# Optimization experiments

Hardware: AMD Instinct MI355X
Metric: run time of the kernel (lower is better)

## Reference

```python
import jax, jax.numpy as jnp
import numpy as np

B, CIN, CMID, COUT, H, W = 4, 64, 128, 128, 128, 128
K = 9  # 3x3 taps
EPS = 1e-5


def conv3x3(x, w, b):
    # standard 3x3 conv, stride 1, pad 1, NCHW / OIHW
    y = jax.lax.conv_general_dilated(x, w, (1, 1), ((1, 1), (1, 1)),
                                     dimension_numbers=('NCHW', 'OIHW', 'NCHW'))
    return y + b[None, :, None, None]


def deform_conv3x3(x, offset, w, b):
    # torchvision DeformConv2d semantics (v1, no mask), kernel 3, pad 1, stride 1.
    # offset: [B, 2*K, H, W] with per-tap (dy, dx) pairs.
    Bn, C, Hn, Wn = x.shape
    off = offset.reshape(Bn, K, 2, Hn, Wn)
    off_y, off_x = off[:, :, 0], off[:, :, 1]          # [B,K,H,W]
    ky = (jnp.arange(K) // 3).astype(x.dtype)          # tap row 0..2
    kx = (jnp.arange(K) % 3).astype(x.dtype)           # tap col 0..2
    # sampling positions: p = out_pos - pad + tap + offset
    py = jnp.arange(Hn, dtype=x.dtype)[None, None, :, None] - 1.0 + ky[None, :, None, None] + off_y
    px = jnp.arange(Wn, dtype=x.dtype)[None, None, None, :] - 1.0 + kx[None, :, None, None] + off_x
    y0 = jnp.floor(py); x0 = jnp.floor(px)
    wy1 = py - y0; wx1 = px - x0                       # bilinear fractions
    y0i = y0.astype(jnp.int32); x0i = x0.astype(jnp.int32)
    xf = x.reshape(Bn, C, Hn * Wn)

    def gather(iy, ix):
        valid = ((iy >= 0) & (iy < Hn) & (ix >= 0) & (ix < Wn)).astype(x.dtype)
        idx = jnp.clip(iy, 0, Hn - 1) * Wn + jnp.clip(ix, 0, Wn - 1)  # [B,K,H,W]
        g = jax.vmap(lambda xb, ib: xb[:, ib])(xf, idx)               # [B,C,K,H,W]
        return g, valid

    g00, v00 = gather(y0i, x0i)
    g01, v01 = gather(y0i, x0i + 1)
    g10, v10 = gather(y0i + 1, x0i)
    g11, v11 = gather(y0i + 1, x0i + 1)

    def wmul(g, v, wgt):
        return g * (v * wgt)[:, None]                  # broadcast over channel dim

    sampled = (wmul(g00, v00, (1 - wy1) * (1 - wx1)) +
               wmul(g01, v01, (1 - wy1) * wx1) +
               wmul(g10, v10, wy1 * (1 - wx1)) +
               wmul(g11, v11, wy1 * wx1))              # [B,C,K,H,W]
    out = jnp.einsum('bckhw,ock->bohw', sampled, w.reshape(w.shape[0], C, K))
    return out + b[None, :, None, None]


def batchnorm_relu(x, gamma, beta):
    # training-mode BN: batch statistics over (N,H,W), biased variance
    mean = jnp.mean(x, axis=(0, 2, 3), keepdims=True)
    var = jnp.mean(jnp.square(x - mean), axis=(0, 2, 3), keepdims=True)
    y = (x - mean) * jax.lax.rsqrt(var + EPS)
    return jax.nn.relu(y * gamma[None, :, None, None] + beta[None, :, None, None])


def setup_inputs() -> dict:
    key = jax.random.key(0)
    ks = jax.random.split(key, 13)
    s = 0.05  # small weights keep offsets small / sampling mostly in-bounds
    return {
        'x': jax.random.normal(ks[0], (B, CIN, H, W), jnp.float32),
        'w_off1': jax.random.normal(ks[1], (2 * K, CIN, 3, 3), jnp.float32) * s,
        'b_off1': jnp.zeros((2 * K,), jnp.float32),
        'w1': jax.random.normal(ks[2], (CMID, CIN, 3, 3), jnp.float32) * s,
        'b1': jax.random.normal(ks[3], (CMID,), jnp.float32) * s,
        'g1': jnp.ones((CMID,), jnp.float32),
        'be1': jnp.zeros((CMID,), jnp.float32),
        'w_off2': jax.random.normal(ks[4], (2 * K, CMID, 3, 3), jnp.float32) * s,
        'b_off2': jnp.zeros((2 * K,), jnp.float32),
        'w2': jax.random.normal(ks[5], (COUT, CMID, 3, 3), jnp.float32) * s,
        'b2': jax.random.normal(ks[6], (COUT,), jnp.float32) * s,
        'g2': jnp.ones((COUT,), jnp.float32),
        'be2': jnp.zeros((COUT,), jnp.float32),
    }


def reference(x, w_off1, b_off1, w1, b1, g1, be1, w_off2, b_off2, w2, b2, g2, be2):
    offset1 = conv3x3(x, w_off1, b_off1)
    out = deform_conv3x3(x, offset1, w1, b1)
    out = batchnorm_relu(out, g1, be1)
    offset2 = conv3x3(out, w_off2, b_off2)
    out = deform_conv3x3(out, offset2, w2, b2)
    out = batchnorm_relu(out, g2, be2)
    return out
```

## Files before the change

kernel.cpp:

```cpp
#include <hip/hip_runtime.h>
#include <hip/hip_bf16.h>

#define BB 4
#define H_ 128
#define W_ 128
#define HWP 16384
#define CIN1 64
#define CMID 128
#define KOFF 18

typedef short short8 __attribute__((ext_vector_type(8)));
typedef float floatx4 __attribute__((ext_vector_type(4)));

#define WS_AB   16
#define WS_CVT  288
#define CVT_TOTAL 4447396
#define WS_WF1  4447744
#define WS_WF2  4484608
#define WS_XT   4558336
#define WS_Y1   7835136
#define WS_Y1T  16223744
#define WS_XTL  18320896
#define WS_WFO1 20418048
#define WS_WFO2 20436480
#define WS_PART 21600000
#define WS_Y2   WS_Y1

#define R_X     0
#define R_WOFF1 4194304
#define R_BOFF1 4204672
#define R_W1    4204690
#define R_B1    4278418
#define R_G1    4278546
#define R_BE1   4278674
#define R_WOFF2 4278802
#define R_BOFF2 4299538
#define R_W2    4299556
#define R_B2    4447012
#define R_G2    4447140
#define R_BE2   4447268

struct SrcPtrs { const void* p[13]; };

__device__ inline short f2bf(float f) {
    __hip_bfloat16 h = __float2bfloat16(f);
    return *reinterpret_cast<short*>(&h);
}
__device__ inline float bf2f(unsigned short u) {
    return __uint_as_float(((unsigned int)u) << 16);
}
__device__ inline float bfu_lo(unsigned int u) { return __uint_as_float(u << 16); }
__device__ inline float bfu_hi(unsigned int u) { return __uint_as_float(u & 0xFFFF0000u); }
__device__ inline float rl_f(float v, int i) {
    return __int_as_float(__builtin_amdgcn_readlane(__float_as_int(v), i));
}

__global__ void probe_dtype_k(const unsigned int* __restrict__ g1, int* __restrict__ flag) {
    if (threadIdx.x == 0 && blockIdx.x == 0) {
        flag[0] = ((g1[0] & 0xFFFFu) != 0u) ? 1 : 0;
    }
}

__global__ __launch_bounds__(256) void convert_inputs_k(SrcPtrs sp, float* __restrict__ dst,
                                                        const int* __restrict__ flag, int total) {
    int i = blockIdx.x * 256 + threadIdx.x;
    if (i >= total) return;
    constexpr int prefix[13] = {0, R_WOFF1, R_BOFF1, R_W1, R_B1, R_G1, R_BE1,
                                R_WOFF2, R_BOFF2, R_W2, R_B2, R_G2, R_BE2};
    const void* src = sp.p[0];
    int base = 0;
#pragma unroll
    for (int q = 1; q < 13; ++q) {
        if (i >= prefix[q]) { src = sp.p[q]; base = prefix[q]; }
    }
    int local = i - base;
    float v;
    if (flag[0] != 0) {
        v = bf2f(((const unsigned short*)src)[local]);
    } else {
        v = ((const float*)src)[local];
    }
    dst[i] = v;
}

template <int CIN>
__global__ __launch_bounds__(256) void wf_build_k(const float* __restrict__ w, short* __restrict__ wf) {
    constexpr int KSTEPS = CIN * 9 / 32;
    int idx = blockIdx.x * 256 + threadIdx.x;
    int j    = idx & 7;
    int lane = (idx >> 3) & 63;
    int rem  = idx >> 9;
    int ks   = rem % KSTEPS;
    int ct   = rem / KSTEPS;
    int co = ct * 16 + (lane & 15);
    int k  = ks * 32 + (lane >> 4) * 8 + j;
    int ci = k & (CIN - 1);
    int kk = k / CIN;
    wf[idx] = f2bf(w[(co * CIN + ci) * 9 + kk]);
}

template <int CIN>
__global__ __launch_bounds__(256) void wf_off_build_k(const float* __restrict__ w, short* __restrict__ wf) {
    constexpr int KSTEPS = CIN * 9 / 32;
    int idx = blockIdx.x * 256 + threadIdx.x;
    int j    = idx & 7;
    int lane = (idx >> 3) & 63;
    int rem  = idx >> 9;
    int ks   = rem % KSTEPS;
    int cc   = rem / KSTEPS;
    int sel  = cc >> 1;
    int co = (cc & 1) * 16 + (lane & 15);
    int k  = ks * 32 + (lane >> 4) * 8 + j;
    int ci = k & (CIN - 1);
    int kk = k / CIN;
    float v = (co < KOFF) ? w[(co * CIN + ci) * 9 + kk] : 0.f;
    short hi = f2bf(v);
    wf[idx] = sel ? f2bf(v - bf2f((unsigned short)hi)) : hi;
}

__global__ __launch_bounds__(256) void xt_build_k(const float* __restrict__ x,
                                                  unsigned short* __restrict__ xt,
                                                  unsigned short* __restrict__ xtl) {
    __shared__ __align__(4) short s_t[64 * 66];
    __shared__ __align__(4) short s_tl[64 * 66];
    int bi  = blockIdx.x;
    int hw0 = (bi & 255) * 64;
    int b   = bi >> 8;
    int t   = threadIdx.x;
    int hwp = t & 63;
#pragma unroll
    for (int it = 0; it < 16; ++it) {
        int c = it * 4 + (t >> 6);
        float v = x[((long)(b * 64 + c) << 14) + hw0 + hwp];
        short hi = f2bf(v);
        s_t[hwp * 66 + c]  = hi;
        s_tl[hwp * 66 + c] = f2bf(v - bf2f((unsigned short)hi));
    }
    __syncthreads();
#pragma unroll
    for (int it = 0; it < 8; ++it) {
        int i  = it * 256 + t;
        int c2 = (i & 31) * 2;
        int hw2 = i >> 5;
        long da = ((long)((b << 14) + hw0 + hw2)) * 64 + c2;
        *(int*)&xt[da]  = *(const int*)&s_t[hw2 * 66 + c2];
        *(int*)&xtl[da] = *(const int*)&s_tl[hw2 * 66 + c2];
    }
}

__device__ inline int conv_tpk(int h, int w0, int lane, int wv) {
    int tpk = 0;
    if (lane < 36) {
        int r = wv + 8 * lane;
        int p = r & 31;
        int k = r >> 5;
        int y = h - 1 + k / 3;
        int x = w0 + p - 1 + (k % 3);
        int valid = (y >= 0 && y < H_ && x >= 0 && x < W_) ? 1 : 0;
        int yc = min(max(y, 0), H_ - 1), xc = min(max(x, 0), W_ - 1);
        tpk = (yc * W_ + xc) | (valid << 16);
    }
    return tpk;
}

__device__ inline void convgather64(const unsigned short* __restrict__ xb, short* __restrict__ s_samp,
                                    int half, int li, int wv, int tpk) {
    constexpr int PADc = 584;
    unsigned int ub[18];
#pragma unroll
    for (int j = 0; j < 18; ++j) {
        int pkA = __builtin_amdgcn_readlane(tpk, 2 * j);
        int pkB = __builtin_amdgcn_readlane(tpk, 2 * j + 1);
        int pk = half ? pkB : pkA;
        unsigned int u = *(const unsigned int*)(xb + (pk & 0xFFFF) * 64 + 2 * li);
        ub[j] = (pk >> 16) ? u : 0u;
    }
#pragma unroll
    for (int j = 0; j < 18; ++j) {
        int r = wv + 8 * (half ? (2 * j + 1) : (2 * j));
        *(unsigned int*)&s_samp[(r & 31) * PADc + (r >> 5) * 64 + 2 * li] = ub[j];
    }
}

template <int I0, int NJ, int KKB>
__device__ inline void convgather128(const unsigned short* __restrict__ xb, short* __restrict__ s_samp,
                                     int lane, int wv, int tpk) {
    constexpr int PADc = 648;
    unsigned int ub[NJ];
#pragma unroll
    for (int j = 0; j < NJ; ++j) {
        int pk = __builtin_amdgcn_readlane(tpk, I0 + j);
        unsigned int u = *(const unsigned int*)(xb + (pk & 0xFFFF) * 128 + 2 * lane);
        ub[j] = (pk >> 16) ? u : 0u;
    }
#pragma unroll
    for (int j = 0; j < NJ; ++j) {
        int r = wv + 8 * (I0 + j);
        *(unsigned int*)&s_samp[(r & 31) * PADc + ((r >> 5) - KKB) * 128 + 2 * lane] = ub[j];
    }
}

__device__ inline void build_table2_lds(const float* __restrict__ s_off,
                                        int h, int w0, int lane, int wv,
                                        int& tpk, float& tw0, float& tw1, float& tw2, float& tw3) {
    tpk = 0; tw0 = tw1 = tw2 = tw3 = 0.f;
    if (lane < 36) {
        int r = wv + 8 * lane;
        int p = r & 31;
        int k = r >> 5;
        int wpix = w0 + p;
        float oy = s_off[(2 * k) * 32 + p];
        float ox = s_off[(2 * k + 1) * 32 + p];
        float py = (float)(h - 1 + (k / 3)) + oy;
        float px = (float)(wpix - 1 + (k % 3)) + ox;
        float fy = floorf(py), fx = floorf(px);
        float wy = py - fy, wx = px - fx;
        int y0 = (int)fy, x0 = (int)fx;
        int y1 = y0 + 1, x1 = x0 + 1;
        bool vy0 = (y0 >= 0) && (y0 < H_);
        bool vy1 = (y1 >= 0) && (y1 < H_);
        bool vx0 = (x0 >= 0) && (x0 < W_);
        bool vx1 = (x1 >= 0) && (x1 < W_);
        float wy0 = 1.f - wy, wx0 = 1.f - wx;
        tw0 = (vy0 && vx0) ? wy0 * wx0 : 0.f;
        tw1 = (vy0 && vx1) ? wy0 * wx  : 0.f;
        tw2 = (vy1 && vx0) ? wy  * wx0 : 0.f;
        tw3 = (vy1 && vx1) ? wy  * wx  : 0.f;
        int iy0 = min(max(y0, 0), H_ - 1), iy1 = min(max(y1, 0), H_ - 1);
        int ix0 = min(max(x0, 0), W_ - 1), ix1 = min(max(x1, 0), W_ - 1);
        int dx = ix1 - ix0;
        int dy = iy1 - iy0;
        tpk = (iy0 * W_ + ix0) | (dx << 14) | (dy << 15);
    }
}

template <int NB>
__device__ inline void gather_batch128v2(const unsigned short* __restrict__ xb, short* __restrict__ s_samp,
                                         int i0, int kkbase, int wv, int lane,
                                         int tpk, float tw0, float tw1, float tw2, float tw3) {
    constexpr int PADc = 648;
    uint4 ub[NB];
#pragma unroll
    for (int j = 0; j < NB; ++j) {
        int pk = __builtin_amdgcn_readlane(tpk, i0 + j);
        const unsigned short* b00 = xb + (pk & 0x3FFF) * 128;
        const unsigned short* b01 = b00 + ((pk >> 14) & 1) * 128;
        const unsigned short* b10 = b00 + ((pk >> 15) & 1) * (W_ * 128);
        const unsigned short* b11 = b01 + ((pk >> 15) & 1) * (W_ * 128);
        ub[j].x = *(const unsigned int*)(b00 + 2 * lane);
        ub[j].y = *(const unsigned int*)(b01 + 2 * lane);
        ub[j].z = *(const unsigned int*)(b10 + 2 * lane);
        ub[j].w = *(const unsigned int*)(b11 + 2 * lane);
    }
#pragma unroll
    for (int j = 0; j < NB; ++j) {
        int i = i0 + j;
        int r = wv + 8 * i;
        float w00 = rl_f(tw0, i), w01 = rl_f(tw1, i), w10 = rl_f(tw2, i), w11 = rl_f(tw3, i);
        float vlo = w00 * bfu_lo(ub[j].x) + w01 * bfu_lo(ub[j].y)
                  + w10 * bfu_lo(ub[j].z) + w11 * bfu_lo(ub[j].w);
        float vhi = w00 * bfu_hi(ub[j].x) + w01 * bfu_hi(ub[j].y)
                  + w10 * bfu_hi(ub[j].z) + w11 * bfu_hi(ub[j].w);
        __hip_bfloat162 h2 = __float22bfloat162_rn(make_float2(vlo, vhi));
        *(unsigned int*)&s_samp[(r & 31) * PADc + ((r >> 5) - kkbase) * 128 + 2 * lane] =
            *reinterpret_cast<unsigned int*>(&h2);
    }
}

template <int NBP>
__device__ inline void gather_batch64v2(const unsigned short* __restrict__ xb, short* __restrict__ s_samp,
                                        int i0, int wv, int half, int li,
                                        int tpk, float tw0, float tw1, float tw2, float tw3) {
    constexpr int PADc = 584;
    uint4 ub[NBP];
#pragma unroll
    for (int j = 0; j < NBP; ++j) {
        int iA = i0 + 2 * j, iB = iA + 1;
        int pkA = __builtin_amdgcn_readlane(tpk, iA);
        int pkB = __builtin_amdgcn_readlane(tpk, iB);
        int pk = half ? pkB : pkA;
        const unsigned short* b00 = xb + (pk & 0x3FFF) * 64;
        const unsigned short* b01 = b00 + ((pk >> 14) & 1) * 64;
        const unsigned short* b10 = b00 + ((pk >> 15) & 1) * (W_ * 64);
        const unsigned short* b11 = b01 + ((pk >> 15) & 1) * (W_ * 64);
        ub[j].x = *(const unsigned int*)(b00 + 2 * li);
        ub[j].y = *(const unsigned int*)(b01 + 2 * li);
        ub[j].z = *(const unsigned int*)(b10 + 2 * li);
        ub[j].w = *(const unsigned int*)(b11 + 2 * li);
    }
#pragma unroll
    for (int j = 0; j < NBP; ++j) {
        int iA = i0 + 2 * j, iB = iA + 1;
        float w00 = half ? rl_f(tw0, iB) : rl_f(tw0, iA);
        float w01 = half ? rl_f(tw1, iB) : rl_f(tw1, iA);
        float w10 = half ? rl_f(tw2, iB) : rl_f(tw2, iA);
        float w11 = half ? rl_f(tw3, iB) : rl_f(tw3, iA);
        float vlo = w00 * bfu_lo(ub[j].x) + w01 * bfu_lo(ub[j].y)
                  + w10 * bfu_lo(ub[j].z) + w11 * bfu_lo(ub[j].w);
        float vhi = w00 * bfu_hi(ub[j].x) + w01 * bfu_hi(ub[j].y)
                  + w10 * bfu_hi(ub[j].z) + w11 * bfu_hi(ub[j].w);
        __hip_bfloat162 h2 = __float22bfloat162_rn(make_float2(vlo, vhi));
        int r = wv + 8 * (half ? iB : iA);
        *(unsigned int*)&s_samp[(r & 31) * PADc + (r >> 5) * 64 + 2 * li] =
            *reinterpret_cast<unsigned int*>(&h2);
    }
}

__global__ __launch_bounds__(512, 4) void fused64_k(const unsigned short* __restrict__ xt,
                                                    const unsigned short* __restrict__ xtl,
                                                    const short* __restrict__ wfo,
                                                    const float* __restrict__ boff,
                                                    const short* __restrict__ wf,
                                                    const float* __restrict__ bias,
                                                    float* __restrict__ out) {
    constexpr int KSTEPS = 18;
    constexpr int PADc = 584;
    __shared__ __align__(16) short s_samp[32 * PADc];
    __shared__ float s_red[4 * 256];
    __shared__ float s_off[KOFF * 32];

    int bi = blockIdx.x;
    int w0 = (bi & 3) * 32;
    int h  = (bi >> 2) & 127;
    int b  = bi >> 9;
    int t  = threadIdx.x;
    int lane = t & 63;
    int wv   = t >> 6;

    const unsigned short* xbh = xt  + (long)b * HWP * 64;
    const unsigned short* xbl = xtl + (long)b * HWP * 64;
    int half = lane >> 5, li = lane & 31;
    int p_   = lane & 15;
    int quad = lane >> 4;

    {
        int tpkc = conv_tpk(h, w0, lane, wv);
        int c   = wv & 3;
        int ksl = wv >> 2;
        int ct  = c & 1;
        int pt  = c >> 1;
        int row = pt * 16 + p_;
        floatx4 acc;
#pragma unroll
        for (int r = 0; r < 4; ++r) {
            int co = ct * 16 + quad * 4 + r;
            acc[r] = (ksl == 0 && co < KOFF) ? boff[co] : 0.f;
        }

        convgather64(xbh, s_samp, half, li, wv, tpkc);
        __syncthreads();
#pragma unroll
        for (int ki = 0; ki < 9; ++ki) {
            int ks = ksl * 9 + ki;
            short8 bfr = *(const short8*)&s_samp[row * PADc + ks * 32 + quad * 8];
            short8 ah  = *(const short8*)&wfo[(((long)ct * KSTEPS + ks) * 64 + lane) * 8];
            short8 al  = *(const short8*)&wfo[(((long)(2 + ct) * KSTEPS + ks) * 64 + lane) * 8];
            acc = __builtin_amdgcn_mfma_f32_16x16x32_bf16(ah, bfr, acc, 0, 0, 0);
            acc = __builtin_amdgcn_mfma_f32_16x16x32_bf16(al, bfr, acc, 0, 0, 0);
        }
        __syncthreads();

        convgather64(xbl, s_samp, half, li, wv, tpkc);
        __syncthreads();
#pragma unroll
        for (int ki = 0; ki < 9; ++ki) {
            int ks = ksl * 9 + ki;
            short8 bfr = *(const short8*)&s_samp[row * PADc + ks * 32 + quad * 8];
            short8 ah  = *(const short8*)&wfo[(((long)ct * KSTEPS + ks) * 64 + lane) * 8];
            acc = __builtin_amdgcn_mfma_f32_16x16x32_bf16(ah, bfr, acc, 0, 0, 0);
        }

        if (ksl == 1) {
#pragma unroll
            for (int r = 0; r < 4; ++r) s_red[c * 256 + (quad * 4 + r) * 16 + p_] = acc[r];
        }
        __syncthreads();
        if (ksl == 0) {
#pragma unroll
            for (int r = 0; r < 4; ++r) {
                int co = ct * 16 + quad * 4 + r;
                if (co < KOFF) {
                    s_off[co * 32 + pt * 16 + p_] = acc[r] + s_red[c * 256 + (quad * 4 + r) * 16 + p_];
                }
            }
        }
        __syncthreads();
    }

    int tpk; float tw0, tw1, tw2, tw3;
    build_table2_lds(s_off, h, w0, lane, wv, tpk, tw0, tw1, tw2, tw3);

    gather_batch64v2<6>(xbh, s_samp,  0, wv, half, li, tpk, tw0, tw1, tw2, tw3);
    gather_batch64v2<6>(xbh, s_samp, 12, wv, half, li, tpk, tw0, tw1, tw2, tw3);
    gather_batch64v2<6>(xbh, s_samp, 24, wv, half, li, tpk, tw0, tw1, tw2, tw3);
    __syncthreads();

    int ct = wv;
    floatx4 acc0, acc1;
#pragma unroll
    for (int r = 0; r < 4; ++r) {
        float bv = bias[ct * 16 + quad * 4 + r];
        acc0[r] = bv;
        acc1[r] = bv;
    }
#pragma unroll 3
    for (int ks = 0; ks < KSTEPS; ++ks) {
        short8 a  = *(const short8*)&wf[(((long)ct * KSTEPS + ks) * 64 + lane) * 8];
        short8 b0 = *(const short8*)&s_samp[p_ * PADc + ks * 32 + quad * 8];
        short8 b1 = *(const short8*)&s_samp[(16 + p_) * PADc + ks * 32 + quad * 8];
        acc0 = __builtin_amdgcn_mfma_f32_16x16x32_bf16(a, b0, acc0, 0, 0, 0);
        acc1 = __builtin_amdgcn_mfma_f32_16x16x32_bf16(a, b1, acc1, 0, 0, 0);
    }

    long ob = ((long)(b * 128) << 14) + (h << 7) + w0 + p_;
#pragma unroll
    for (int r = 0; r < 4; ++r) {
        long cpl = (long)(ct * 16 + quad * 4 + r) << 14;
        out[ob + cpl]      = acc0[r];
        out[ob + 16 + cpl] = acc1[r];
    }
}

__global__ __launch_bounds__(512, 4) void fused128_k(const unsigned short* __restrict__ xt,
                                                     const unsigned short* __restrict__ xtl,
                                                     const short* __restrict__ wfo,
                                                     const float* __restrict__ boff,
                                                     const short* __restrict__ wf,
                                                     const float* __restrict__ bias,
                                                     float* __restrict__ out) {
    constexpr int KSTEPS = 36;
    constexpr int PADc = 648;
    __shared__ __align__(16) short s_samp[32 * PADc];
    __shared__ float s_red[4 * 256];
    __shared__ float s_off[KOFF * 32];

    int bi = blockIdx.x;
    int w0 = (bi & 3) * 32;
    int h  = (bi >> 2) & 127;
    int b  = bi >> 9;
    int t  = threadIdx.x;
    int lane = t & 63;
    int wv   = t >> 6;

    const unsigned short* xbh = xt  + (long)b * HWP * 128;
    const unsigned short* xbl = xtl + (long)b * HWP * 128;
    int p_   = lane & 15;
    int quad = lane >> 4;

    {
        int tpkc = conv_tpk(h, w0, lane, wv);
        int c   = wv & 3;
        int ksl = wv >> 2;
        int ct  = c & 1;
        int pt  = c >> 1;
        int row = pt * 16 + p_;
        floatx4 acc;
#pragma unroll
        for (int r = 0; r < 4; ++r) {
            int co = ct * 16 + quad * 4 + r;
            acc[r] = (ksl == 0 && co < KOFF) ? boff[co] : 0.f;
        }

        convgather128<0, 16, 0>(xbh, s_samp, lane, wv, tpkc);
        __syncthreads();
#pragma unroll
        for (int ki = 0; ki < 8; ++ki) {
            int ks = ksl * 8 + ki;
            short8 bfr = *(const short8*)&s_samp[row * PADc + ks * 32 + quad * 8];
            short8 ah  = *(const short8*)&wfo[(((long)ct * KSTEPS + ks) * 64 + lane) * 8];
            short8 al  = *(const short8*)&wfo[(((long)(2 + ct) * KSTEPS + ks) * 64 + lane) * 8];
            acc = __builtin_amdgcn_mfma_f32_16x16x32_bf16(ah, bfr, acc, 0, 0, 0);
            acc = __builtin_amdgcn_mfma_f32_16x16x32_bf16(al, bfr, acc, 0, 0, 0);
        }
        __syncthreads();

        convgather128<16, 20, 4>(xbh, s_samp, lane, wv, tpkc);
        __syncthreads();
#pragma unroll
        for (int ki = 0; ki < 10; ++ki) {
            int ks = 16 + ksl * 10 + ki;
            short8 bfr = *(const short8*)&s_samp[row * PADc + (ks - 16) * 32 + quad * 8];
            short8 ah  = *(const short8*)&wfo[(((long)ct * KSTEPS + ks) * 64 + lane) * 8];
            short8 al  = *(const short8*)&wfo[(((long)(2 + ct) * KSTEPS + ks) * 64 + lane) * 8];
            acc = __builtin_amdgcn_mfma_f32_16x16x32_bf16(ah, bfr, acc, 0, 0, 0);
            acc = __builtin_amdgcn_mfma_f32_16x16x32_bf16(al, bfr, acc, 0, 0, 0);
        }
        __syncthreads();

        convgather128<0, 16, 0>(xbl, s_samp, lane, wv, tpkc);
        __syncthreads();
#pragma unroll
        for (int ki = 0; ki < 8; ++ki) {
            int ks = ksl * 8 + ki;
            short8 bfr = *(const short8*)&s_samp[row * PADc + ks * 32 + quad * 8];
            short8 ah  = *(const short8*)&wfo[(((long)ct * KSTEPS + ks) * 64 + lane) * 8];
            acc = __builtin_amdgcn_mfma_f32_16x16x32_bf16(ah, bfr, acc, 0, 0, 0);
        }
        __syncthreads();

        convgather128<16, 20, 4>(xbl, s_samp, lane, wv, tpkc);
        __syncthreads();
#pragma unroll
        for (int ki = 0; ki < 10; ++ki) {
            int ks = 16 + ksl * 10 + ki;
            short8 bfr = *(const short8*)&s_samp[row * PADc + (ks - 16) * 32 + quad * 8];
            short8 ah  = *(const short8*)&wfo[(((long)ct * KSTEPS + ks) * 64 + lane) * 8];
            acc = __builtin_amdgcn_mfma_f32_16x16x32_bf16(ah, bfr, acc, 0, 0, 0);
        }

        if (ksl == 1) {
#pragma unroll
            for (int r = 0; r < 4; ++r) s_red[c * 256 + (quad * 4 + r) * 16 + p_] = acc[r];
        }
        __syncthreads();
        if (ksl == 0) {
#pragma unroll
            for (int r = 0; r < 4; ++r) {
                int co = ct * 16 + quad * 4 + r;
                if (co < KOFF) {
                    s_off[co * 32 + pt * 16 + p_] = acc[r] + s_red[c * 256 + (quad * 4 + r) * 16 + p_];
                }
            }
        }
        __syncthreads();
    }

    int tpk; float tw0, tw1, tw2, tw3;
    build_table2_lds(s_off, h, w0, lane, wv, tpk, tw0, tw1, tw2, tw3);

    int ct = wv;
    floatx4 acc0, acc1;
#pragma unroll
    for (int r = 0; r < 4; ++r) {
        float bv = bias[ct * 16 + quad * 4 + r];
        acc0[r] = bv;
        acc1[r] = bv;
    }

    gather_batch128v2<8>(xbh, s_samp, 0, 0, wv, lane, tpk, tw0, tw1, tw2, tw3);
    gather_batch128v2<8>(xbh, s_samp, 8, 0, wv, lane, tpk, tw0, tw1, tw2, tw3);
    __syncthreads();
#pragma unroll 4
    for (int ks = 0; ks < 16; ++ks) {
        short8 a  = *(const short8*)&wf[(((long)ct * KSTEPS + ks) * 64 + lane) * 8];
        short8 b0 = *(const short8*)&s_samp[p_ * PADc + ks * 32 + quad * 8];
        short8 b1 = *(const short8*)&s_samp[(16 + p_) * PADc + ks * 32 + quad * 8];
        acc0 = __builtin_amdgcn_mfma_f32_16x16x32_bf16(a, b0, acc0, 0, 0, 0);
        acc1 = __builtin_amdgcn_mfma_f32_16x16x32_bf16(a, b1, acc1, 0, 0, 0);
    }
    __syncthreads();

    gather_batch128v2<5>(xbh, s_samp, 16, 4, wv, lane, tpk, tw0, tw1, tw2, tw3);
    gather_batch128v2<5>(xbh, s_samp, 21, 4, wv, lane, tpk, tw0, tw1, tw2, tw3);
    gather_batch128v2<5>(xbh, s_samp, 26, 4, wv, lane, tpk, tw0, tw1, tw2, tw3);
    gather_batch128v2<5>(xbh, s_samp, 31, 4, wv, lane, tpk, tw0, tw1, tw2, tw3);
    __syncthreads();
#pragma unroll 4
    for (int ks = 16; ks < KSTEPS; ++ks) {
        short8 a  = *(const short8*)&wf[(((long)ct * KSTEPS + ks) * 64 + lane) * 8];
        short8 b0 = *(const short8*)&s_samp[p_ * PADc + (ks - 16) * 32 + quad * 8];
        short8 b1 = *(const short8*)&s_samp[(16 + p_) * PADc + (ks - 16) * 32 + quad * 8];
        acc0 = __builtin_amdgcn_mfma_f32_16x16x32_bf16(a, b0, acc0, 0, 0, 0);
        acc1 = __builtin_amdgcn_mfma_f32_16x16x32_bf16(a, b1, acc1, 0, 0, 0);
    }

    long ob = ((long)(b * 128) << 14) + (h << 7) + w0 + p_;
#pragma unroll
    for (int r = 0; r < 4; ++r) {
        long cpl = (long)(ct * 16 + quad * 4 + r) << 14;
        out[ob + cpl]      = acc0[r];
        out[ob + 16 + cpl] = acc1[r];
    }
}

__global__ __launch_bounds__(256) void bn_stats_part_k(const float* __restrict__ y, float* __restrict__ part) {
    int bi = blockIdx.x;
    int c = bi & 127;
    int b = bi >> 7;
    int t = threadIdx.x;
    const float4* p4 = (const float4*)(y + ((long)(b * 128 + c) << 14));
    float sum = 0.f, ss = 0.f;
#pragma unroll
    for (int i = 0; i < 16; ++i) {
        float4 v = p4[t + 256 * i];
        sum += v.x + v.y + v.z + v.w;
        ss  += v.x * v.x + v.y * v.y + v.z * v.z + v.w * v.w;
    }
#pragma unroll
    for (int o = 32; o > 0; o >>= 1) { sum += __shfl_down(sum, o); ss += __shfl_down(ss, o); }
    __shared__ float s1[4], s2[4];
    int wave = t >> 6;
    if ((t & 63) == 0) { s1[wave] = sum; s2[wave] = ss; }
    __syncthreads();
    if (t == 0) {
        part[bi]       = s1[0] + s1[1] + s1[2] + s1[3];
        part[512 + bi] = s2[0] + s2[1] + s2[2] + s2[3];
    }
}

__global__ __launch_bounds__(256) void bn_apply_dual_k(float* __restrict__ y, const float* __restrict__ part,
                                                       const float* __restrict__ g, const float* __restrict__ be,
                                                       unsigned short* __restrict__ yt,
                                                       unsigned short* __restrict__ ytl) {
    __shared__ __align__(4) short s_t[64 * 134];
    __shared__ __align__(4) short s_tl[64 * 134];
    __shared__ float s_a[128], s_sh[128];
    int t = threadIdx.x;
    if (t < 128) {
        float sum = part[t] + part[128 + t] + part[256 + t] + part[384 + t];
        float ss  = part[512 + t] + part[640 + t] + part[768 + t] + part[896 + t];
        float mean = sum * (1.f / 65536.f);
        float var  = ss  * (1.f / 65536.f) - mean * mean;
        float inv  = rsqrtf(var + 1e-5f);
        float a = g[t] * inv;
        s_a[t]  = a;
        s_sh[t] = be[t] - mean * a;
    }
    __syncthreads();

    int bi  = blockIdx.x;
    int hw0 = (bi & 255) * 64;
    int b   = bi >> 8;
    int hwp = t & 63;
#pragma unroll 4
    for (int it = 0; it < 32; ++it) {
        int c = it * 4 + (t >> 6);
        float a = s_a[c], sh = s_sh[c];
        long addr = ((long)(b * 128 + c) << 14) + hw0 + hwp;
        float v = y[addr];
        v = fmaxf(v * a + sh, 0.f);
        y[addr] = v;
        short hi = f2bf(v);
        s_t[hwp * 134 + c]  = hi;
        s_tl[hwp * 134 + c] = f2bf(v - bf2f((unsigned short)hi));
    }
    __syncthreads();
#pragma unroll 4
    for (int it = 0; it < 16; ++it) {
        int i   = it * 256 + t;
        int c2  = (i & 63) * 2;
        int hw2 = i >> 6;
        long da = ((long)((b << 14) + hw0 + hw2)) * 128 + c2;
        *(int*)&yt[da]  = *(const int*)&s_t[hw2 * 134 + c2];
        *(int*)&ytl[da] = *(const int*)&s_tl[hw2 * 134 + c2];
    }
}

__global__ __launch_bounds__(256) void bn_apply_out_k(const float* __restrict__ y, const float* __restrict__ part,
                                                      const float* __restrict__ g, const float* __restrict__ be,
                                                      const int* __restrict__ flag, void* __restrict__ out, int total4) {
    __shared__ float s_a[128], s_sh[128];
    int t = threadIdx.x;
    if (t < 128) {
        float sum = part[t] + part[128 + t] + part[256 + t] + part[384 + t];
        float ss  = part[512 + t] + part[640 + t] + part[768 + t] + part[896 + t];
        float mean = sum * (1.f / 65536.f);
        float var  = ss  * (1.f / 65536.f) - mean * mean;
        float inv  = rsqrtf(var + 1e-5f);
        float a = g[t] * inv;
        s_a[t]  = a;
        s_sh[t] = be[t] - mean * a;
    }
    __syncthreads();

    int i = blockIdx.x * 256 + t;
    if (i >= total4) return;
    int c = (i >> 12) & 127;
    float a = s_a[c], sh = s_sh[c];
    float4 v = reinterpret_cast<const float4*>(y)[i];
    v.x = fmaxf(v.x * a + sh, 0.f);
    v.y = fmaxf(v.y * a + sh, 0.f);
    v.z = fmaxf(v.z * a + sh, 0.f);
    v.w = fmaxf(v.w * a + sh, 0.f);
    if (flag[0] != 0) {
        ushort4 u;
        u.x = (unsigned short)f2bf(v.x);
        u.y = (unsigned short)f2bf(v.y);
        u.z = (unsigned short)f2bf(v.z);
        u.w = (unsigned short)f2bf(v.w);
        reinterpret_cast<ushort4*>(out)[i] = u;
    } else {
        reinterpret_cast<float4*>(out)[i] = v;
    }
}

extern "C" void kernel_launch(void* const* d_in, const int* in_sizes, int n_in,
                              void* d_out, int out_size, void* d_ws, size_t ws_size,
                              hipStream_t stream) {
    float* ws   = (float*)d_ws;
    int*   flag = (int*)d_ws;
    float* cvt  = ws + WS_CVT;

    const float* X     = cvt + R_X;
    const float* Woff1 = cvt + R_WOFF1;
    const float* Boff1 = cvt + R_BOFF1;
    const float* W1f   = cvt + R_W1;
    const float* B1f   = cvt + R_B1;
    const float* G1    = cvt + R_G1;
    const float* Be1   = cvt + R_BE1;
    const float* Woff2 = cvt + R_WOFF2;
    const float* Boff2 = cvt + R_BOFF2;
    const float* W2f   = cvt + R_W2;
    const float* B2f   = cvt + R_B2;
    const float* G2    = cvt + R_G2;
    const float* Be2   = cvt + R_BE2;

    short* WF1  = (short*)(ws + WS_WF1);
    short* WF2  = (short*)(ws + WS_WF2);
    short* WFO1 = (short*)(ws + WS_WFO1);
    short* WFO2 = (short*)(ws + WS_WFO2);
    unsigned short* XT   = (unsigned short*)(ws + WS_XT);
    unsigned short* XTL  = (unsigned short*)(ws + WS_XTL);
    unsigned short* Y1T  = (unsigned short*)(ws + WS_Y1T);
    unsigned short* Y1TL = (unsigned short*)(ws + WS_CVT);
    float* PART = ws + WS_PART;
    float* Y1   = ws + WS_Y1;
    float* Y2   = ws + WS_Y2;

    SrcPtrs sp;
    for (int j = 0; j < 13; ++j) sp.p[j] = d_in[j];

    probe_dtype_k<<<1, 64, 0, stream>>>((const unsigned int*)d_in[5], flag);
    convert_inputs_k<<<(CVT_TOTAL + 255) / 256, 256, 0, stream>>>(sp, cvt, flag, CVT_TOTAL);
    wf_build_k<64><<<288, 256, 0, stream>>>(W1f, WF1);
    wf_build_k<128><<<576, 256, 0, stream>>>(W2f, WF2);
    wf_off_build_k<64><<<144, 256, 0, stream>>>(Woff1, WFO1);
    wf_off_build_k<128><<<288, 256, 0, stream>>>(Woff2, WFO2);
    xt_build_k<<<1024, 256, 0, stream>>>(X, XT, XTL);

    fused64_k<<<BB * 128 * 4, 512, 0, stream>>>(XT, XTL, WFO1, Boff1, WF1, B1f, Y1);
    bn_stats_part_k<<<512, 256, 0, stream>>>(Y1, PART);
    bn_apply_dual_k<<<1024, 256, 0, stream>>>(Y1, PART, G1, Be1, Y1T, Y1TL);

    fused128_k<<<BB * 128 * 4, 512, 0, stream>>>(Y1T, Y1TL, WFO2, Boff2, WF2, B2f, Y2);
    bn_stats_part_k<<<512, 256, 0, stream>>>(Y2, PART);
    bn_apply_out_k<<<(BB * 128 * HWP / 4 + 255) / 256, 256, 0, stream>>>(Y2, PART, G2, Be2, flag, d_out, BB * 128 * HWP / 4);
}
```

Baseline: 330.8 us.

## Fuse BN statistics into deform-conv epilogues and shrink LDS tiles for occupancy

Drops the separate BN statistics kernels. Each fused conv kernel now reduces per-channel sum and sum-of-squares with wave shuffles and accumulates them into a zeroed partials buffer via atomics. The K dimension of the staged samples is split into smaller chunks (PADc 520), so LDS per block shrinks and launch bounds can request 8 blocks per CU. It also removes the unused write-back of normalized Y1. The costs are extra syncs and gather phases, plus atomic contention on 256 addresses.

```diff
diff --git a/kernel.cpp b/kernel.cpp
--- a/kernel.cpp
+++ b/kernel.cpp
@@ -5,8 +5,6 @@
 #define H_ 128
 #define W_ 128
 #define HWP 16384
-#define CIN1 64
-#define CMID 128
 #define KOFF 18
 
 typedef short short8 __attribute__((ext_vector_type(8)));
@@ -163,29 +161,32 @@
     return tpk;
 }
 
+template <int J0, int NJ, int KKB>
 __device__ inline void convgather64(const unsigned short* __restrict__ xb, short* __restrict__ s_samp,
                                     int half, int li, int wv, int tpk) {
-    constexpr int PADc = 584;
-    unsigned int ub[18];
-#pragma unroll
-    for (int j = 0; j < 18; ++j) {
-        int pkA = __builtin_amdgcn_readlane(tpk, 2 * j);
-        int pkB = __builtin_amdgcn_readlane(tpk, 2 * j + 1);
+    constexpr int PADc = 520;
+    unsigned int ub[NJ];
+#pragma unroll
+    for (int j = 0; j < NJ; ++j) {
+        int jj = J0 + j;
+        int pkA = __builtin_amdgcn_readlane(tpk, 2 * jj);
+        int pkB = __builtin_amdgcn_readlane(tpk, 2 * jj + 1);
         int pk = half ? pkB : pkA;
         unsigned int u = *(const unsigned int*)(xb + (pk & 0xFFFF) * 64 + 2 * li);
         ub[j] = (pk >> 16) ? u : 0u;
     }
 #pragma unroll
-    for (int j = 0; j < 18; ++j) {
-        int r = wv + 8 * (half ? (2 * j + 1) : (2 * j));
-        *(unsigned int*)&s_samp[(r & 31) * PADc + (r >> 5) * 64 + 2 * li] = ub[j];
+    for (int j = 0; j < NJ; ++j) {
+        int jj = J0 + j;
+        int r = wv + 8 * (half ? (2 * jj + 1) : (2 * jj));
+        *(unsigned int*)&s_samp[(r & 31) * PADc + ((r >> 5) - KKB) * 64 + 2 * li] = ub[j];
     }
 }
 
 template <int I0, int NJ, int KKB>
 __device__ inline void convgather128(const unsigned short* __restrict__ xb, short* __restrict__ s_samp,
                                      int lane, int wv, int tpk) {
-    constexpr int PADc = 648;
+    constexpr int PADc = 520;
     unsigned int ub[NJ];
 #pragma unroll
     for (int j = 0; j < NJ; ++j) {
@@ -238,7 +239,7 @@
 __device__ inline void gather_batch128v2(const unsigned short* __restrict__ xb, short* __restrict__ s_samp,
                                          int i0, int kkbase, int wv, int lane,
                                          int tpk, float tw0, float tw1, float tw2, float tw3) {
-    constexpr int PADc = 648;
+    constexpr int PADc = 520;
     uint4 ub[NB];
 #pragma unroll
     for (int j = 0; j < NB; ++j) {
@@ -269,9 +270,9 @@
 
 template <int NBP>
 __device__ inline void gather_batch64v2(const unsigned short* __restrict__ xb, short* __restrict__ s_samp,
-                                        int i0, int wv, int half, int li,
+                                        int i0, int kkbase, int wv, int half, int li,
                                         int tpk, float tw0, float tw1, float tw2, float tw3) {
-    constexpr int PADc = 584;
+    constexpr int PADc = 520;
     uint4 ub[NBP];
 #pragma unroll
     for (int j = 0; j < NBP; ++j) {
@@ -301,20 +302,36 @@
                   + w10 * bfu_hi(ub[j].z) + w11 * bfu_hi(ub[j].w);
         __hip_bfloat162 h2 = __float22bfloat162_rn(make_float2(vlo, vhi));
         int r = wv + 8 * (half ? iB : iA);
-        *(unsigned int*)&s_samp[(r & 31) * PADc + (r >> 5) * 64 + 2 * li] =
+        *(unsigned int*)&s_samp[(r & 31) * PADc + ((r >> 5) - kkbase) * 64 + 2 * li] =
             *reinterpret_cast<unsigned int*>(&h2);
     }
 }
 
-__global__ __launch_bounds__(512, 4) void fused64_k(const unsigned short* __restrict__ xt,
+__device__ inline void bn_epilogue(floatx4 acc0, floatx4 acc1, int ct, int quad, int p_,
+                                   float* __restrict__ part) {
+#pragma unroll
+    for (int r = 0; r < 4; ++r) {
+        float sm = acc0[r] + acc1[r];
+        float sq = acc0[r] * acc0[r] + acc1[r] * acc1[r];
+#pragma unroll
+        for (int o = 1; o < 16; o <<= 1) { sm += __shfl_xor(sm, o); sq += __shfl_xor(sq, o); }
+        if (p_ == 0) {
+            int co = ct * 16 + quad * 4 + r;
+            atomicAdd(&part[co], sm);
+            atomicAdd(&part[512 + co], sq);
+        }
+    }
+}
+
+__global__ __launch_bounds__(512, 8) void fused64_k(const unsigned short* __restrict__ xt,
                                                     const unsigned short* __restrict__ xtl,
                                                     const short* __restrict__ wfo,
                                                     const float* __restrict__ boff,
                                                     const short* __restrict__ wf,
                                                     const float* __restrict__ bias,
-                                                    float* __restrict__ out) {
-    constexpr int KSTEPS = 18;
-    constexpr int PADc = 584;
+                                                    float* __restrict__ out,
+                                                    float* __restrict__ part) {
+    constexpr int PADc = 520;
     __shared__ __align__(16) short s_samp[32 * PADc];
     __shared__ float s_red[4 * 256];
     __shared__ float s_off[KOFF * 32];
@@ -347,26 +364,48 @@
             acc[r] = (ksl == 0 && co < KOFF) ? boff[co] : 0.f;
         }
 
-        convgather64(xbh, s_samp, half, li, wv, tpkc);
-        __syncthreads();
-#pragma unroll
-        for (int ki = 0; ki < 9; ++ki) {
-            int ks = ksl * 9 + ki;
+        convgather64<0, 16, 0>(xbh, s_samp, half, li, wv, tpkc);
+        __syncthreads();
+#pragma unroll
+        for (int ki = 0; ki < 8; ++ki) {
+            int ks = ksl * 8 + ki;
             short8 bfr = *(const short8*)&s_samp[row * PADc + ks * 32 + quad * 8];
-            short8 ah  = *(const short8*)&wfo[(((long)ct * KSTEPS + ks) * 64 + lane) * 8];
-            short8 al  = *(const short8*)&wfo[(((long)(2 + ct) * KSTEPS + ks) * 64 + lane) * 8];
+            short8 ah  = *(const short8*)&wfo[(((long)ct * 18 + ks) * 64 + lane) * 8];
+            short8 al  = *(const short8*)&wfo[(((long)(2 + ct) * 18 + ks) * 64 + lane) * 8];
             acc = __builtin_amdgcn_mfma_f32_16x16x32_bf16(ah, bfr, acc, 0, 0, 0);
             acc = __builtin_amdgcn_mfma_f32_16x16x32_bf16(al, bfr, acc, 0, 0, 0);
         }
         __syncthreads();
 
-        convgather64(xbl, s_samp, half, li, wv, tpkc);
-        __syncthreads();
-#pragma unroll
-        for (int ki = 0; ki < 9; ++ki) {
-            int ks = ksl * 9 + ki;
+        convgather64<16, 2, 8>(xbh, s_samp, half, li, wv, tpkc);
+        __syncthreads();
+        {
+            int ks = 16 + ksl;
+            short8 bfr = *(const short8*)&s_samp[row * PADc + (ks - 16) * 32 + quad * 8];
+            short8 ah  = *(const short8*)&wfo[(((long)ct * 18 + ks) * 64 + lane) * 8];
+            short8 al  = *(const short8*)&wfo[(((long)(2 + ct) * 18 + ks) * 64 + lane) * 8];
+            acc = __builtin_amdgcn_mfma_f32_16x16x32_bf16(ah, bfr, acc, 0, 0, 0);
+            acc = __builtin_amdgcn_mfma_f32_16x16x32_bf16(al, bfr, acc, 0, 0, 0);
+        }
+        __syncthreads();
+
+        convgather64<0, 16, 0>(xbl, s_samp, half, li, wv, tpkc);
+        __syncthreads();
+#pragma unroll
+        for (int ki = 0; ki < 8; ++ki) {
+            int ks = ksl * 8 + ki;
             short8 bfr = *(const short8*)&s_samp[row * PADc + ks * 32 + quad * 8];
-            short8 ah  = *(const short8*)&wfo[(((long)ct * KSTEPS + ks) * 64 + lane) * 8];
+            short8 ah  = *(const short8*)&wfo[(((long)ct * 18 + ks) * 64 + lane) * 8];
+            acc = __builtin_amdgcn_mfma_f32_16x16x32_bf16(ah, bfr, acc, 0, 0, 0);
+        }
+        __syncthreads();
+
+        convgather64<16, 2, 8>(xbl, s_samp, half, li, wv, tpkc);
+        __syncthreads();
+        {
+            int ks = 16 + ksl;
+            short8 bfr = *(const short8*)&s_samp[row * PADc + (ks - 16) * 32 + quad * 8];
+            short8 ah  = *(const short8*)&wfo[(((long)ct * 18 + ks) * 64 + lane) * 8];
             acc = __builtin_amdgcn_mfma_f32_16x16x32_bf16(ah, bfr, acc, 0, 0, 0);
         }
 
@@ -390,11 +429,6 @@
     int tpk; float tw0, tw1, tw2, tw3;
     build_table2_lds(s_off, h, w0, lane, wv, tpk, tw0, tw1, tw2, tw3);
 
-    gather_batch64v2<6>(xbh, s_samp,  0, wv, half, li, tpk, tw0, tw1, tw2, tw3);
-    gather_batch64v2<6>(xbh, s_samp, 12, wv, half, li, tpk, tw0, tw1, tw2, tw3);
-    gather_batch64v2<6>(xbh, s_samp, 24, wv, half, li, tpk, tw0, tw1, tw2, tw3);
-    __syncthreads();
-
     int ct = wv;
     floatx4 acc0, acc1;
 #pragma unroll
@@ -403,14 +437,30 @@
         acc0[r] = bv;
         acc1[r] = bv;
     }
-#pragma unroll 3
-    for (int ks = 0; ks < KSTEPS; ++ks) {
-        short8 a  = *(const short8*)&wf[(((long)ct * KSTEPS + ks) * 64 + lane) * 8];
+
+    gather_batch64v2<8>(xbh, s_samp,  0, 0, wv, half, li, tpk, tw0, tw1, tw2, tw3);
+    gather_batch64v2<8>(xbh, s_samp, 16, 0, wv, half, li, tpk, tw0, tw1, tw2, tw3);
+    __syncthreads();
+#pragma unroll 4
+    for (int ks = 0; ks < 16; ++ks) {
+        short8 a  = *(const short8*)&wf[(((long)ct * 18 + ks) * 64 + lane) * 8];
         short8 b0 = *(const short8*)&s_samp[p_ * PADc + ks * 32 + quad * 8];
         short8 b1 = *(const short8*)&s_samp[(16 + p_) * PADc + ks * 32 + quad * 8];
         acc0 = __builtin_amdgcn_mfma_f32_16x16x32_bf16(a, b0, acc0, 0, 0, 0);
         acc1 = __builtin_amdgcn_mfma_f32_16x16x32_bf16(a, b1, acc1, 0, 0, 0);
     }
+    __syncthreads();
+
+    gather_batch64v2<2>(xbh, s_samp, 32, 8, wv, half, li, tpk, tw0, tw1, tw2, tw3);
+    __syncthreads();
+#pragma unroll
+    for (int ks = 16; ks < 18; ++ks) {
+        short8 a  = *(const short8*)&wf[(((long)ct * 18 + ks) * 64 + lane) * 8];
+        short8 b0 = *(const short8*)&s_samp[p_ * PADc + (ks - 16) * 32 + quad * 8];
+        short8 b1 = *(const short8*)&s_samp[(16 + p_) * PADc + (ks - 16) * 32 + quad * 8];
+        acc0 = __builtin_amdgcn_mfma_f32_16x16x32_bf16(a, b0, acc0, 0, 0, 0);
+        acc1 = __builtin_amdgcn_mfma_f32_16x16x32_bf16(a, b1, acc1, 0, 0, 0);
+    }
 
     long ob = ((long)(b * 128) << 14) + (h << 7) + w0 + p_;
 #pragma unroll
@@ -419,17 +469,18 @@
         out[ob + cpl]      = acc0[r];
         out[ob + 16 + cpl] = acc1[r];
     }
-}
-
-__global__ __launch_bounds__(512, 4) void fused128_k(const unsigned short* __restrict__ xt,
+    bn_epilogue(acc0, acc1, ct, quad, p_, part);
+}
+
+__global__ __launch_bounds__(512, 8) void fused128_k(const unsigned short* __restrict__ xt,
                                                      const unsigned short* __restrict__ xtl,
                                                      const short* __restrict__ wfo,
                                                      const float* __restrict__ boff,
                                                      const short* __restrict__ wf,
                                                      const float* __restrict__ bias,
-                                                     float* __restrict__ out) {
-    constexpr int KSTEPS = 36;
-    constexpr int PADc = 648;
+                                                     float* __restrict__ out,
+                                                     float* __restrict__ part) {
+    constexpr int PADc = 520;
     __shared__ __align__(16) short s_samp[32 * PADc];
     __shared__ float s_red[4 * 256];
     __shared__ float s_off[KOFF * 32];
@@ -467,21 +518,34 @@
         for (int ki = 0; ki < 8; ++ki) {
             int ks = ksl * 8 + ki;
             short8 bfr = *(const short8*)&s_samp[row * PADc + ks * 32 + quad * 8];
-            short8 ah  = *(const short8*)&wfo[(((long)ct * KSTEPS + ks) * 64 + lane) * 8];
-            short8 al  = *(const short8*)&wfo[(((long)(2 + ct) * KSTEPS + ks) * 64 + lane) * 8];
+            short8 ah  = *(const short8*)&wfo[(((long)ct * 36 + ks) * 64 + lane) * 8];
+            short8 al  = *(const short8*)&wfo[(((long)(2 + ct) * 36 + ks) * 64 + lane) * 8];
             acc = __builtin_amdgcn_mfma_f32_16x16x32_bf16(ah, bfr, acc, 0, 0, 0);
             acc = __builtin_amdgcn_mfma_f32_16x16x32_bf16(al, bfr, acc, 0, 0, 0);
         }
         __syncthreads();
 
-        convgather128<16, 20, 4>(xbh, s_samp, lane, wv, tpkc);
-        __syncthreads();
-#pragma unroll
-        for (int ki = 0; ki < 10; ++ki) {
-            int ks = 16 + ksl * 10 + ki;
+        convgather128<16, 16, 4>(xbh, s_samp, lane, wv, tpkc);
+        __syncthreads();
+#pragma unroll
+        for (int ki = 0; ki < 8; ++ki) {
+            int ks = 16 + ksl * 8 + ki;
             short8 bfr = *(const short8*)&s_samp[row * PADc + (ks - 16) * 32 + quad * 8];
-            short8 ah  = *(const short8*)&wfo[(((long)ct * KSTEPS + ks) * 64 + lane) * 8];
-            short8 al  = *(const short8*)&wfo[(((long)(2 + ct) * KSTEPS + ks) * 64 + lane) * 8];
+            short8 ah  = *(const short8*)&wfo[(((long)ct * 36 + ks) * 64 + lane) * 8];
+            short8 al  = *(const short8*)&wfo[(((long)(2 + ct) * 36 + ks) * 64 + lane) * 8];
+            acc = __builtin_amdgcn_mfma_f32_16x16x32_bf16(ah, bfr, acc, 0, 0, 0);
+            acc = __builtin_amdgcn_mfma_f32_16x16x32_bf16(al, bfr, acc, 0, 0, 0);
+        }
+        __syncthreads();
+
+        convgather128<32, 4, 8>(xbh, s_samp, lane, wv, tpkc);
+        __syncthreads();
+#pragma unroll
+        for (int ki = 0; ki < 2; ++ki) {
+            int ks = 32 + ksl * 2 + ki;
+            short8 bfr = *(const short8*)&s_samp[row * PADc + (ks - 32) * 32 + quad * 8];
+            short8 ah  = *(const short8*)&wfo[(((long)ct * 36 + ks) * 64 + lane) * 8];
+            short8 al  = *(const short8*)&wfo[(((long)(2 + ct) * 36 + ks) * 64 + lane) * 8];
             acc = __builtin_amdgcn_mfma_f32_16x16x32_bf16(ah, bfr, acc, 0, 0, 0);
             acc = __builtin_amdgcn_mfma_f32_16x16x32_bf16(al, bfr, acc, 0, 0, 0);
         }
@@ -493,18 +557,29 @@
         for (int ki = 0; ki < 8; ++ki) {
             int ks = ksl * 8 + ki;
             short8 bfr = *(const short8*)&s_samp[row * PADc + ks * 32 + quad * 8];
-            short8 ah  = *(const short8*)&wfo[(((long)ct * KSTEPS + ks) * 64 + lane) * 8];
-            acc = __builtin_amdgcn_mfma_f32_16x16x32_bf16(ah, bfr, acc, 0, 0, 0);
-        }
-        __syncthreads();
-
-        convgather128<16, 20, 4>(xbl, s_samp, lane, wv, tpkc);
-        __syncthreads();
-#pragma unroll
-        for (int ki = 0; ki < 10; ++ki) {
-            int ks = 16 + ksl * 10 + ki;
+            short8 ah  = *(const short8*)&wfo[(((long)ct * 36 + ks) * 64 + lane) * 8];
+            acc = __builtin_amdgcn_mfma_f32_16x16x32_bf16(ah, bfr, acc, 0, 0, 0);
+        }
+        __syncthreads();
+
+        convgather128<16, 16, 4>(xbl, s_samp, lane, wv, tpkc);
+        __syncthreads();
+#pragma unroll
+        for (int ki = 0; ki < 8; ++ki) {
+            int ks = 16 + ksl * 8 + ki;
             short8 bfr = *(const short8*)&s_samp[row * PADc + (ks - 16) * 32 + quad * 8];
-            short8 ah  = *(const short8*)&wfo[(((long)ct * KSTEPS + ks) * 64 + lane) * 8];
+            short8 ah  = *(const short8*)&wfo[(((long)ct * 36 + ks) * 64 + lane) * 8];
+            acc = __builtin_amdgcn_mfma_f32_16x16x32_bf16(ah, bfr, acc, 0, 0, 0);
+        }
+        __syncthreads();
+
+        convgather128<32, 4, 8>(xbl, s_samp, lane, wv, tpkc);
+        __syncthreads();
+#pragma unroll
+        for (int ki = 0; ki < 2; ++ki) {
+            int ks = 32 + ksl * 2 + ki;
+            short8 bfr = *(const short8*)&s_samp[row * PADc + (ks - 32) * 32 + quad * 8];
+            short8 ah  = *(const short8*)&wfo[(((long)ct * 36 + ks) * 64 + lane) * 8];
             acc = __builtin_amdgcn_mfma_f32_16x16x32_bf16(ah, bfr, acc, 0, 0, 0);
         }
 
@@ -542,7 +617,7 @@
     __syncthreads();
 #pragma unroll 4
     for (int ks = 0; ks < 16; ++ks) {
-        short8 a  = *(const short8*)&wf[(((long)ct * KSTEPS + ks) * 64 + lane) * 8];
+        short8 a  = *(const short8*)&wf[(((long)ct * 36 + ks) * 64 + lane) * 8];
         short8 b0 = *(const short8*)&s_samp[p_ * PADc + ks * 32 + quad * 8];
         short8 b1 = *(const short8*)&s_samp[(16 + p_) * PADc + ks * 32 + quad * 8];
         acc0 = __builtin_amdgcn_mfma_f32_16x16x32_bf16(a, b0, acc0, 0, 0, 0);
@@ -550,19 +625,29 @@
     }
     __syncthreads();
 
-    gather_batch128v2<5>(xbh, s_samp, 16, 4, wv, lane, tpk, tw0, tw1, tw2, tw3);
-    gather_batch128v2<5>(xbh, s_samp, 21, 4, wv, lane, tpk, tw0, tw1, tw2, tw3);
-    gather_batch128v2<5>(xbh, s_samp, 26, 4, wv, lane, tpk, tw0, tw1, tw2, tw3);
-    gather_batch128v2<5>(xbh, s_samp, 31, 4, wv, lane, tpk, tw0, tw1, tw2, tw3);
+    gather_batch128v2<8>(xbh, s_samp, 16, 4, wv, lane, tpk, tw0, tw1, tw2, tw3);
+    gather_batch128v2<8>(xbh, s_samp, 24, 4, wv, lane, tpk, tw0, tw1, tw2, tw3);
     __syncthreads();
 #pragma unroll 4
-    for (int ks = 16; ks < KSTEPS; ++ks) {
-        short8 a  = *(const short8*)&wf[(((long)ct * KSTEPS + ks) * 64 + lane) * 8];
+    for (int ks = 16; ks < 32; ++ks) {
+        short8 a  = *(const short8*)&wf[(((long)ct * 36 + ks) * 64 + lane) * 8];
         short8 b0 = *(const short8*)&s_samp[p_ * PADc + (ks - 16) * 32 + quad * 8];
         short8 b1 = *(const short8*)&s_samp[(16 + p_) * PADc + (ks - 16) * 32 + quad * 8];
         acc0 = __builtin_amdgcn_mfma_f32_16x16x32_bf16(a, b0, acc0, 0, 0, 0);
         acc1 = __builtin_amdgcn_mfma_f32_16x16x32_bf16(a, b1, acc1, 0, 0, 0);
     }
+    __syncthreads();
+
+    gather_batch128v2<4>(xbh, s_samp, 32, 8, wv, lane, tpk, tw0, tw1, tw2, tw3);
+    __syncthreads();
+#pragma unroll
+    for (int ks = 32; ks < 36; ++ks) {
+        short8 a  = *(const short8*)&wf[(((long)ct * 36 + ks) * 64 + lane) * 8];
+        short8 b0 = *(const short8*)&s_samp[p_ * PADc + (ks - 32) * 32 + quad * 8];
+        short8 b1 = *(const short8*)&s_samp[(16 + p_) * PADc + (ks - 32) * 32 + quad * 8];
+        acc0 = __builtin_amdgcn_mfma_f32_16x16x32_bf16(a, b0, acc0, 0, 0, 0);
+        acc1 = __builtin_amdgcn_mfma_f32_16x16x32_bf16(a, b1, acc1, 0, 0, 0);
+    }
 
     long ob = ((long)(b * 128) << 14) + (h << 7) + w0 + p_;
 #pragma unroll
@@ -571,34 +656,10 @@
         out[ob + cpl]      = acc0[r];
         out[ob + 16 + cpl] = acc1[r];
     }
-}
-
-__global__ __launch_bounds__(256) void bn_stats_part_k(const float* __restrict__ y, float* __restrict__ part) {
-    int bi = blockIdx.x;
-    int c = bi & 127;
-    int b = bi >> 7;
-    int t = threadIdx.x;
-    const float4* p4 = (const float4*)(y + ((long)(b * 128 + c) << 14));
-    float sum = 0.f, ss = 0.f;
-#pragma unroll
-    for (int i = 0; i < 16; ++i) {
-        float4 v = p4[t + 256 * i];
-        sum += v.x + v.y + v.z + v.w;
-        ss  += v.x * v.x + v.y * v.y + v.z * v.z + v.w * v.w;
-    }
-#pragma unroll
-    for (int o = 32; o > 0; o >>= 1) { sum += __shfl_down(sum, o); ss += __shfl_down(ss, o); }
-    __shared__ float s1[4], s2[4];
-    int wave = t >> 6;
-    if ((t & 63) == 0) { s1[wave] = sum; s2[wave] = ss; }
-    __syncthreads();
-    if (t == 0) {
-        part[bi]       = s1[0] + s1[1] + s1[2] + s1[3];
-        part[512 + bi] = s2[0] + s2[1] + s2[2] + s2[3];
-    }
-}
-
-__global__ __launch_bounds__(256) void bn_apply_dual_k(float* __restrict__ y, const float* __restrict__ part,
+    bn_epilogue(acc0, acc1, ct, quad, p_, part);
+}
+
+__global__ __launch_bounds__(256) void bn_apply_dual_k(const float* __restrict__ y, const float* __restrict__ part,
                                                        const float* __restrict__ g, const float* __restrict__ be,
                                                        unsigned short* __restrict__ yt,
                                                        unsigned short* __restrict__ ytl) {
@@ -629,7 +690,6 @@
         long addr = ((long)(b * 128 + c) << 14) + hw0 + hwp;
         float v = y[addr];
         v = fmaxf(v * a + sh, 0.f);
-        y[addr] = v;
         short hi = f2bf(v);
         s_t[hwp * 134 + c]  = hi;
         s_tl[hwp * 134 + c] = f2bf(v - bf2f((unsigned short)hi));
@@ -728,11 +788,11 @@
     wf_off_build_k<128><<<288, 256, 0, stream>>>(Woff2, WFO2);
     xt_build_k<<<1024, 256, 0, stream>>>(X, XT, XTL);
 
-    fused64_k<<<BB * 128 * 4, 512, 0, stream>>>(XT, XTL, WFO1, Boff1, WF1, B1f, Y1);
-    bn_stats_part_k<<<512, 256, 0, stream>>>(Y1, PART);
+    hipMemsetAsync(PART, 0, 1024 * sizeof(float), stream);
+    fused64_k<<<BB * 128 * 4, 512, 0, stream>>>(XT, XTL, WFO1, Boff1, WF1, B1f, Y1, PART);
     bn_apply_dual_k<<<1024, 256, 0, stream>>>(Y1, PART, G1, Be1, Y1T, Y1TL);
 
-    fused128_k<<<BB * 128 * 4, 512, 0, stream>>>(Y1T, Y1TL, WFO2, Boff2, WF2, B2f, Y2);
-    bn_stats_part_k<<<512, 256, 0, stream>>>(Y2, PART);
+    hipMemsetAsync(PART, 0, 1024 * sizeof(float), stream);
+    fused128_k<<<BB * 128 * 4, 512, 0, stream>>>(Y1T, Y1TL, WFO2, Boff2, WF2, B2f, Y2, PART);
     bn_apply_out_k<<<(BB * 128 * HWP / 4 + 255) / 256, 256, 0, stream>>>(Y2, PART, G2, Be2, flag, d_out, BB * 128 * HWP / 4);
 }
```

After: 638.5 us. 93.0% more time.

## Prefetch next conv gather into registers during MFMA and drop redundant BN writeback

Applied to the files above, without the earlier changes.

The offset-conv gather is split into separate global-load and LDS-store helpers. Each stage's loads for the next slab, the low-part split or the second tap group, are issued into registers before the MFMA loop on the current slab, then written to LDS after the barrier. This hides gather latency behind matrix work, at the cost of more live registers and possibly lower occupancy. Separately, bn_apply_dual_k no longer writes the normalized fp32 activation back to y, since only the bf16 hi/lo transposed copies appear to be consumed.

```diff
diff --git a/kernel.cpp b/kernel.cpp
--- a/kernel.cpp
+++ b/kernel.cpp
@@ -5,8 +5,6 @@
 #define H_ 128
 #define W_ 128
 #define HWP 16384
-#define CIN1 64
-#define CMID 128
 #define KOFF 18
 
 typedef short short8 __attribute__((ext_vector_type(8)));
@@ -163,36 +161,40 @@
     return tpk;
 }
 
-__device__ inline void convgather64(const unsigned short* __restrict__ xb, short* __restrict__ s_samp,
-                                    int half, int li, int wv, int tpk) {
-    constexpr int PADc = 584;
-    unsigned int ub[18];
-#pragma unroll
-    for (int j = 0; j < 18; ++j) {
+template <int NJ>
+__device__ inline void conv_load64(const unsigned short* __restrict__ xb, unsigned int* ub,
+                                   int half, int li, int tpk) {
+#pragma unroll
+    for (int j = 0; j < NJ; ++j) {
         int pkA = __builtin_amdgcn_readlane(tpk, 2 * j);
         int pkB = __builtin_amdgcn_readlane(tpk, 2 * j + 1);
         int pk = half ? pkB : pkA;
         unsigned int u = *(const unsigned int*)(xb + (pk & 0xFFFF) * 64 + 2 * li);
         ub[j] = (pk >> 16) ? u : 0u;
     }
-#pragma unroll
-    for (int j = 0; j < 18; ++j) {
+}
+template <int NJ, int PADc>
+__device__ inline void conv_store64(short* __restrict__ s_samp, const unsigned int* ub,
+                                    int half, int li, int wv) {
+#pragma unroll
+    for (int j = 0; j < NJ; ++j) {
         int r = wv + 8 * (half ? (2 * j + 1) : (2 * j));
         *(unsigned int*)&s_samp[(r & 31) * PADc + (r >> 5) * 64 + 2 * li] = ub[j];
     }
 }
-
-template <int I0, int NJ, int KKB>
-__device__ inline void convgather128(const unsigned short* __restrict__ xb, short* __restrict__ s_samp,
-                                     int lane, int wv, int tpk) {
-    constexpr int PADc = 648;
-    unsigned int ub[NJ];
+template <int I0, int NJ>
+__device__ inline void conv_load128(const unsigned short* __restrict__ xb, unsigned int* ub,
+                                    int lane, int tpk) {
 #pragma unroll
     for (int j = 0; j < NJ; ++j) {
         int pk = __builtin_amdgcn_readlane(tpk, I0 + j);
         unsigned int u = *(const unsigned int*)(xb + (pk & 0xFFFF) * 128 + 2 * lane);
         ub[j] = (pk >> 16) ? u : 0u;
     }
+}
+template <int I0, int NJ, int KKB, int PADc>
+__device__ inline void conv_store128(short* __restrict__ s_samp, const unsigned int* ub,
+                                     int wv, int lane) {
 #pragma unroll
     for (int j = 0; j < NJ; ++j) {
         int r = wv + 8 * (I0 + j);
@@ -347,8 +349,14 @@
             acc[r] = (ksl == 0 && co < KOFF) ? boff[co] : 0.f;
         }
 
-        convgather64(xbh, s_samp, half, li, wv, tpkc);
-        __syncthreads();
+        {
+            unsigned int ubh[18];
+            conv_load64<18>(xbh, ubh, half, li, tpkc);
+            conv_store64<18, PADc>(s_samp, ubh, half, li, wv);
+        }
+        __syncthreads();
+        unsigned int ubl[18];
+        conv_load64<18>(xbl, ubl, half, li, tpkc);
 #pragma unroll
         for (int ki = 0; ki < 9; ++ki) {
             int ks = ksl * 9 + ki;
@@ -359,8 +367,7 @@
             acc = __builtin_amdgcn_mfma_f32_16x16x32_bf16(al, bfr, acc, 0, 0, 0);
         }
         __syncthreads();
-
-        convgather64(xbl, s_samp, half, li, wv, tpkc);
+        conv_store64<18, PADc>(s_samp, ubl, half, li, wv);
         __syncthreads();
 #pragma unroll
         for (int ki = 0; ki < 9; ++ki) {
@@ -461,8 +468,11 @@
             acc[r] = (ksl == 0 && co < KOFF) ? boff[co] : 0.f;
         }
 
-        convgather128<0, 16, 0>(xbh, s_samp, lane, wv, tpkc);
-        __syncthreads();
+        unsigned int ubA[16], ubB[20];
+        conv_load128<0, 16>(xbh, ubA, lane, tpkc);
+        conv_store128<0, 16, 0, PADc>(s_samp, ubA, wv, lane);
+        __syncthreads();
+        conv_load128<16, 20>(xbh, ubB, lane, tpkc);
 #pragma unroll
         for (int ki = 0; ki < 8; ++ki) {
             int ks = ksl * 8 + ki;
@@ -473,9 +483,9 @@
             acc = __builtin_amdgcn_mfma_f32_16x16x32_bf16(al, bfr, acc, 0, 0, 0);
         }
         __syncthreads();
-
-        convgather128<16, 20, 4>(xbh, s_samp, lane, wv, tpkc);
-        __syncthreads();
+        conv_store128<16, 20, 4, PADc>(s_samp, ubB, wv, lane);
+        __syncthreads();
+        conv_load128<0, 16>(xbl, ubA, lane, tpkc);
 #pragma unroll
         for (int ki = 0; ki < 10; ++ki) {
             int ks = 16 + ksl * 10 + ki;
@@ -486,9 +496,9 @@
             acc = __builtin_amdgcn_mfma_f32_16x16x32_bf16(al, bfr, acc, 0, 0, 0);
         }
         __syncthreads();
-
-        convgather128<0, 16, 0>(xbl, s_samp, lane, wv, tpkc);
-        __syncthreads();
+        conv_store128<0, 16, 0, PADc>(s_samp, ubA, wv, lane);
+        __syncthreads();
+        conv_load128<16, 20>(xbl, ubB, lane, tpkc);
 #pragma unroll
         for (int ki = 0; ki < 8; ++ki) {
             int ks = ksl * 8 + ki;
@@ -497,8 +507,7 @@
             acc = __builtin_amdgcn_mfma_f32_16x16x32_bf16(ah, bfr, acc, 0, 0, 0);
         }
         __syncthreads();
-
-        convgather128<16, 20, 4>(xbl, s_samp, lane, wv, tpkc);
+        conv_store128<16, 20, 4, PADc>(s_samp, ubB, wv, lane);
         __syncthreads();
 #pragma unroll
         for (int ki = 0; ki < 10; ++ki) {
@@ -598,7 +607,7 @@
     }
 }
 
-__global__ __launch_bounds__(256) void bn_apply_dual_k(float* __restrict__ y, const float* __restrict__ part,
+__global__ __launch_bounds__(256) void bn_apply_dual_k(const float* __restrict__ y, const float* __restrict__ part,
                                                        const float* __restrict__ g, const float* __restrict__ be,
                                                        unsigned short* __restrict__ yt,
                                                        unsigned short* __restrict__ ytl) {
@@ -629,7 +638,6 @@
         long addr = ((long)(b * 128 + c) << 14) + hw0 + hwp;
         float v = y[addr];
         v = fmaxf(v * a + sh, 0.f);
-        y[addr] = v;
         short hi = f2bf(v);
         s_t[hwp * 134 + c]  = hi;
         s_tl[hwp * 134 + c] = f2bf(v - bf2f((unsigned short)hi));
```

Measured after the change: 331.0 us. No clear change (+0.1%).
